# Optimization experiments

Hardware: AMD Instinct MI355X
Metric: run time of the kernel (lower is better)

## Reference

```python
import jax, jax.numpy as jnp
import numpy as np

B, S, H, NH = 8, 2048, 128, 4
HS = H // NH
EPS = 1e-8


def setup_inputs() -> dict:
    key = jax.random.key(0)
    ks = jax.random.split(key, 20)
    sc = 1.0 / np.sqrt(H)
    d = {
        'item_embeds': jax.random.normal(ks[0], (B, S, H), jnp.float32),
        'behavior_embeds': jax.random.normal(ks[1], (B, S, H), jnp.float32),
        'attn_mask': jnp.zeros((B, 1, S, S), jnp.float32),
    }
    names = ['Wq', 'Wk', 'Wv', 'Wqb', 'Wkb', 'Wvb', 'Wf']
    for i, n in enumerate(names):
        d[n] = jax.random.normal(ks[2 + i], (H, H), jnp.float32) * sc
        d['b' + n[1:]] = jnp.zeros((H,), jnp.float32)
    d['ln_w'] = jnp.ones((H,), jnp.float32)
    d['ln_b'] = jnp.zeros((H,), jnp.float32)
    return d


def _split_heads(x):
    # [B,S,H] -> [B,NH,S,HS]
    return x.reshape(B, S, NH, HS).transpose(0, 2, 1, 3)


def _layer_norm(x, w, b):
    u = jnp.mean(x, -1, keepdims=True)
    s = jnp.mean((x - u) ** 2, -1, keepdims=True)
    return w * ((x - u) / jnp.sqrt(s + EPS)) + b


def reference(item_embeds, behavior_embeds, attn_mask,
              Wq, bq, Wk, bk, Wv, bv,
              Wqb, bqb, Wkb, bkb, Wvb, bvb,
              Wf, bf, ln_w, ln_b):
    Q = _split_heads(item_embeds @ Wq + bq)
    K = _split_heads(item_embeds @ Wk + bk)
    V = _split_heads(item_embeds @ Wv + bv)
    Qb = _split_heads(behavior_embeds @ Wqb + bqb)
    Kb = _split_heads(behavior_embeds @ Wkb + bkb)
    # V_behavior computed in the original forward but unused downstream
    _Vb = _split_heads(behavior_embeds @ Wvb + bvb)
    scores = (jnp.einsum('bhqd,bhkd->bhqk', Q, K)
              + jnp.einsum('bhqd,bhkd->bhqk', Qb, Kb)) / np.sqrt(HS)
    scores = scores + attn_mask
    probs = jax.nn.softmax(scores, axis=-1)
    attn_out = jnp.einsum('bhqk,bhkd->bhqd', probs, V)
    attn_out = attn_out.transpose(0, 2, 1, 3).reshape(B, S, H)
    out = attn_out @ Wf + bf
    return _layer_norm(out + item_embeds, ln_w, ln_b)
```

## Files before the change

### kernel.cpp

```cpp
#include <hip/hip_runtime.h>
#include <math.h>

typedef unsigned short ushort_t;
typedef __attribute__((ext_vector_type(8))) short bf16x8;
typedef __attribute__((ext_vector_type(4))) float f32x4;

namespace {
constexpr int B = 8, S = 2048, H = 128, NH = 4, HS = 32;
constexpr float EPS = 1e-8f;
constexpr float SCALE = 0.17677669529663687f;
constexpr int QT = 16, KT = 64;
constexpr int NE = B * S * H;
}

__device__ __forceinline__ ushort_t f2bf(float f) {
  unsigned u = __float_as_uint(f);
  unsigned r = (u + 0x7FFFu + ((u >> 16) & 1u)) >> 16;
  return (ushort_t)r;
}

__device__ __forceinline__ f32x4 mfma16(bf16x8 a, bf16x8 b, f32x4 c) {
  return __builtin_amdgcn_mfma_f32_16x16x32_bf16(a, b, c, 0, 0, 0);
}

__global__ __launch_bounds__(256) void wcvt_kernel(
    const float* __restrict__ Wq, const float* __restrict__ Wk, const float* __restrict__ Wv,
    const float* __restrict__ Wqb, const float* __restrict__ Wkb, const float* __restrict__ Wf,
    ushort_t* __restrict__ Wt)
{
  const float* Ws[6] = {Wq, Wk, Wv, Wqb, Wkb, Wf};
  const float scl[6] = {SCALE, 1.f, 1.f, SCALE, 1.f, 1.f};
  const int m = blockIdx.y;
  const int kb = blockIdx.x;
  const float* W = Ws[m];
  const float sc = scl[m];
  __shared__ float T[32 * 132];
  const int t = threadIdx.x;
#pragma unroll
  for (int u = 0; u < 4; ++u) {
    const int idx = u * 256 + t;
    const int row = idx >> 5, c4 = idx & 31;
    const float4 v = *(const float4*)&W[(kb * 32 + row) * H + c4 * 4];
    *(float4*)&T[row * 132 + c4 * 4] = v;
  }
  __syncthreads();
#pragma unroll
  for (int u = 0; u < 16; ++u) {
    const int idx = u * 256 + t;
    const int n = idx >> 5, kk = idx & 31;
    Wt[m * (H * H) + n * H + kb * 32 + kk] = f2bf(T[kk * 132 + n] * sc);
  }
}

__global__ __launch_bounds__(256) void proj_kernel(
    const float* __restrict__ item, const float* __restrict__ beh,
    const ushort_t* __restrict__ Wt,
    const float* __restrict__ bq, const float* __restrict__ bk, const float* __restrict__ bv,
    const float* __restrict__ bqb, const float* __restrict__ bkb,
    ushort_t* __restrict__ Qo, ushort_t* __restrict__ Ko, ushort_t* __restrict__ Qbo,
    ushort_t* __restrict__ Kbo, ushort_t* __restrict__ Vto)
{
  __shared__ ushort_t Xi[16 * 136];
  __shared__ ushort_t Xb[16 * 136];
  __shared__ ushort_t Yb[5][16 * 136];
  const int t = threadIdx.x;
  const long r0 = (long)blockIdx.x * 16;
#pragma unroll
  for (int u = 0; u < 2; ++u) {
    const int idx = u * 256 + t;
    const int row = idx >> 5, c4 = idx & 31;
    const float4 vi = *(const float4*)&item[(r0 + row) * H + c4 * 4];
    const float4 vb = *(const float4*)&beh[(r0 + row) * H + c4 * 4];
    unsigned long long pi = (unsigned long long)f2bf(vi.x) | ((unsigned long long)f2bf(vi.y) << 16)
        | ((unsigned long long)f2bf(vi.z) << 32) | ((unsigned long long)f2bf(vi.w) << 48);
    unsigned long long pb = (unsigned long long)f2bf(vb.x) | ((unsigned long long)f2bf(vb.y) << 16)
        | ((unsigned long long)f2bf(vb.z) << 32) | ((unsigned long long)f2bf(vb.w) << 48);
    *(unsigned long long*)&Xi[row * 136 + c4 * 4] = pi;
    *(unsigned long long*)&Xb[row * 136 + c4 * 4] = pb;
  }
  __syncthreads();

  const int w = t >> 6, l = t & 63, l15 = l & 15, quad = l >> 4;
  const int bb = (int)(r0 >> 11);
  const int s0 = (int)(r0 & (S - 1));
  const float* bias[5] = {bq, bk, bv, bqb, bkb};
  const float bscale[5] = {SCALE, 1.f, 1.f, SCALE, 1.f};

  bf16x8 afi[4], afb[4];
#pragma unroll
  for (int ks = 0; ks < 4; ++ks) {
    afi[ks] = *(const bf16x8*)&Xi[l15 * 136 + ks * 32 + quad * 8];
    afb[ks] = *(const bf16x8*)&Xb[l15 * 136 + ks * 32 + quad * 8];
  }

#pragma unroll
  for (int p = 0; p < 5; ++p) {
    f32x4 acc[2];
#pragma unroll
    for (int nt = 0; nt < 2; ++nt) {
      const float bcol = bias[p][w * 32 + nt * 16 + l15] * bscale[p];
      acc[nt] = (f32x4){bcol, bcol, bcol, bcol};
    }
    const ushort_t* Wp = Wt + p * (H * H);
    const bf16x8* af = (p < 3) ? afi : afb;
#pragma unroll
    for (int ks = 0; ks < 4; ++ks) {
      bf16x8 bfr[2];
#pragma unroll
      for (int nt = 0; nt < 2; ++nt)
        bfr[nt] = *(const bf16x8*)&Wp[(w * 32 + nt * 16 + l15) * H + ks * 32 + quad * 8];
#pragma unroll
      for (int nt = 0; nt < 2; ++nt)
        acc[nt] = mfma16(af[ks], bfr[nt], acc[nt]);
    }
#pragma unroll
    for (int nt = 0; nt < 2; ++nt)
#pragma unroll
      for (int r = 0; r < 4; ++r)
        Yb[p][(quad * 4 + r) * 136 + w * 32 + nt * 16 + l15] = f2bf(acc[nt][r]);
  }
  __syncthreads();
  {
    const int row = t >> 4, cb = (t & 15) * 8;
    const int h = cb >> 5, dd = cb & 31;
    const long gidx = ((long)(bb * NH + h) * S + s0 + row) * HS + dd;
    ushort_t* dsts4[4] = {Qo, Ko, Qbo, Kbo};
    const int psrc[4] = {0, 1, 3, 4};
#pragma unroll
    for (int i = 0; i < 4; ++i)
      *(uint4*)&dsts4[i][gidx] = *(const uint4*)&Yb[psrc[i]][row * 136 + cb];
    const int d = t >> 1, sh = (t & 1) * 8;
    ushort_t tmp[8];
#pragma unroll
    for (int i = 0; i < 8; ++i) tmp[i] = Yb[2][(sh + i) * 136 + d];
    const long vidx = ((long)(bb * NH + (d >> 5)) * HS + (d & 31)) * S + s0 + sh;
    *(uint4*)&Vto[vidx] = *(const uint4*)&tmp[0];
  }
}

__global__ __launch_bounds__(256, 4) void attn_kernel(
    const ushort_t* __restrict__ Q, const ushort_t* __restrict__ K,
    const ushort_t* __restrict__ Qb, const ushort_t* __restrict__ Kb,
    const ushort_t* __restrict__ Vt, const float* __restrict__ mask,
    ushort_t* __restrict__ attn_out)
{
  __shared__ ushort_t Pb[NH][16 * 72];
  const int t = threadIdx.x;
  const int w = t >> 6;
  const int l = t & 63, l15 = l & 15, quad = l >> 4;
  const int q0 = blockIdx.x * QT;
  const int b = blockIdx.y;
  const long hQ = (long)(b * NH + w) * S * HS;
  const long hV = (long)(b * NH + w) * HS * S;

  const bf16x8 qf  = *(const bf16x8*)&Q[hQ + (long)(q0 + l15) * HS + quad * 8];
  const bf16x8 qbf = *(const bf16x8*)&Qb[hQ + (long)(q0 + l15) * HS + quad * 8];

  const float* mrow[4];
#pragma unroll
  for (int r = 0; r < 4; ++r)
    mrow[r] = mask + ((long)b * S + q0 + quad * 4 + r) * S + l15;

  float lsum[4] = {0.f, 0.f, 0.f, 0.f};
  f32x4 O[2];
#pragma unroll
  for (int dt = 0; dt < 2; ++dt) O[dt] = (f32x4){0.f, 0.f, 0.f, 0.f};
  ushort_t* Pw = Pb[w];

  float msk[4][4];
#pragma unroll
  for (int nt = 0; nt < 4; ++nt)
#pragma unroll
    for (int r = 0; r < 4; ++r)
      msk[nt][r] = mrow[r][nt * 16];

  for (int kt = 0; kt < S / KT; ++kt) {
    const int k0 = kt * KT;
    f32x4 sc[4];
#pragma unroll
    for (int nt = 0; nt < 4; ++nt)
#pragma unroll
      for (int r = 0; r < 4; ++r)
        sc[nt][r] = msk[nt][r];
    if (kt + 1 < S / KT) {
#pragma unroll
      for (int nt = 0; nt < 4; ++nt)
#pragma unroll
        for (int r = 0; r < 4; ++r)
          msk[nt][r] = mrow[r][k0 + KT + nt * 16];
    }
    bf16x8 kf[4], kbf[4], vf[2][2];
#pragma unroll
    for (int nt = 0; nt < 4; ++nt) {
      kf[nt]  = *(const bf16x8*)&K[hQ + (long)(k0 + nt * 16 + l15) * HS + quad * 8];
      kbf[nt] = *(const bf16x8*)&Kb[hQ + (long)(k0 + nt * 16 + l15) * HS + quad * 8];
    }
#pragma unroll
    for (int dt = 0; dt < 2; ++dt)
#pragma unroll
      for (int ks = 0; ks < 2; ++ks)
        vf[dt][ks] = *(const bf16x8*)&Vt[hV + (long)(dt * 16 + l15) * S + k0 + ks * 32 + quad * 8];
#pragma unroll
    for (int nt = 0; nt < 4; ++nt) {
      sc[nt] = mfma16(qbf, kbf[nt], sc[nt]);
      sc[nt] = mfma16(qf, kf[nt], sc[nt]);
    }
#pragma unroll
    for (int nt = 0; nt < 4; ++nt) {
      float ps = 0.f;
#pragma unroll
      for (int r = 0; r < 4; ++r) {
        const float p = __expf(sc[nt][r]);
        sc[nt][r] = p;
      }
      (void)ps;
    }
#pragma unroll
    for (int r = 0; r < 4; ++r)
      lsum[r] += sc[0][r] + sc[1][r] + sc[2][r] + sc[3][r];
#pragma unroll
    for (int nt = 0; nt < 4; ++nt)
#pragma unroll
      for (int r = 0; r < 4; ++r)
        Pw[(quad * 4 + r) * 72 + nt * 16 + l15] = f2bf(sc[nt][r]);
    bf16x8 pf[2];
#pragma unroll
    for (int ks = 0; ks < 2; ++ks)
      pf[ks] = *(const bf16x8*)&Pw[l15 * 72 + ks * 32 + quad * 8];
#pragma unroll
    for (int dt = 0; dt < 2; ++dt)
#pragma unroll
      for (int ks = 0; ks < 2; ++ks)
        O[dt] = mfma16(pf[ks], vf[dt][ks], O[dt]);
  }
#pragma unroll
  for (int r = 0; r < 4; ++r) {
    float s = lsum[r];
    s += __shfl_xor(s, 1);
    s += __shfl_xor(s, 2);
    s += __shfl_xor(s, 4);
    s += __shfl_xor(s, 8);
    lsum[r] = s;
  }
#pragma unroll
  for (int r = 0; r < 4; ++r) {
    const float inv = 1.f / lsum[r];
    const long row = (long)b * S + q0 + quad * 4 + r;
#pragma unroll
    for (int dt = 0; dt < 2; ++dt)
      attn_out[row * H + w * 32 + dt * 16 + l15] = f2bf(O[dt][r] * inv);
  }
}

__global__ __launch_bounds__(256) void out_kernel(
    const ushort_t* __restrict__ attn, const float* __restrict__ item,
    const ushort_t* __restrict__ Wft, const float* __restrict__ bf_,
    const float* __restrict__ lnw, const float* __restrict__ lnb,
    float* __restrict__ out)
{
  __shared__ ushort_t As[16 * 136];
  __shared__ float Ys[16 * 132];
  const int t = threadIdx.x;
  const long r0 = (long)blockIdx.x * 16;
  {
    const int row = t >> 4, c8 = t & 15;
    *(uint4*)&As[row * 136 + c8 * 8] = *(const uint4*)&attn[(r0 + row) * H + c8 * 8];
  }
  __syncthreads();
  const int w = t >> 6, l = t & 63, l15 = l & 15, quad = l >> 4;
  f32x4 acc[2];
#pragma unroll
  for (int nt = 0; nt < 2; ++nt) {
    const float bcol = bf_[w * 32 + nt * 16 + l15];
    acc[nt] = (f32x4){bcol, bcol, bcol, bcol};
  }
#pragma unroll
  for (int ks = 0; ks < 4; ++ks) {
    const bf16x8 a = *(const bf16x8*)&As[l15 * 136 + ks * 32 + quad * 8];
#pragma unroll
    for (int nt = 0; nt < 2; ++nt) {
      const bf16x8 bfr = *(const bf16x8*)&Wft[(w * 32 + nt * 16 + l15) * H + ks * 32 + quad * 8];
      acc[nt] = mfma16(a, bfr, acc[nt]);
    }
  }
#pragma unroll
  for (int nt = 0; nt < 2; ++nt)
#pragma unroll
    for (int r = 0; r < 4; ++r) {
      const int rl = quad * 4 + r;
      const int col = w * 32 + nt * 16 + l15;
      Ys[rl * 132 + col] = acc[nt][r] + item[(r0 + rl) * H + col];
    }
  __syncthreads();
  const int rl = t >> 4, ch = t & 15;
  float v[8];
#pragma unroll
  for (int g = 0; g < 2; ++g) {
    const float4 y = *(const float4*)&Ys[rl * 132 + ch * 8 + g * 4];
    v[g * 4 + 0] = y.x; v[g * 4 + 1] = y.y; v[g * 4 + 2] = y.z; v[g * 4 + 3] = y.w;
  }
  float s = 0.f;
#pragma unroll
  for (int i = 0; i < 8; ++i) s += v[i];
  s += __shfl_xor(s, 1);
  s += __shfl_xor(s, 2);
  s += __shfl_xor(s, 4);
  s += __shfl_xor(s, 8);
  const float u_ = s * (1.f / H);
  float s2 = 0.f;
#pragma unroll
  for (int i = 0; i < 8; ++i) { const float d = v[i] - u_; s2 += d * d; }
  s2 += __shfl_xor(s2, 1);
  s2 += __shfl_xor(s2, 2);
  s2 += __shfl_xor(s2, 4);
  s2 += __shfl_xor(s2, 8);
  const float rinv = rsqrtf(s2 * (1.f / H) + EPS);
#pragma unroll
  for (int g = 0; g < 2; ++g) {
    float4 o;
    const int col = ch * 8 + g * 4;
    o.x = lnw[col + 0] * ((v[g * 4 + 0] - u_) * rinv) + lnb[col + 0];
    o.y = lnw[col + 1] * ((v[g * 4 + 1] - u_) * rinv) + lnb[col + 1];
    o.z = lnw[col + 2] * ((v[g * 4 + 2] - u_) * rinv) + lnb[col + 2];
    o.w = lnw[col + 3] * ((v[g * 4 + 3] - u_) * rinv) + lnb[col + 3];
    *(float4*)&out[(r0 + rl) * H + col] = o;
  }
}

extern "C" void kernel_launch(void* const* d_in, const int* in_sizes, int n_in,
                              void* d_out, int out_size, void* d_ws, size_t ws_size,
                              hipStream_t stream) {
  const float* item = (const float*)d_in[0];
  const float* beh  = (const float*)d_in[1];
  const float* mask = (const float*)d_in[2];
  const float* Wq  = (const float*)d_in[3];  const float* bq  = (const float*)d_in[4];
  const float* Wk  = (const float*)d_in[5];  const float* bk  = (const float*)d_in[6];
  const float* Wv  = (const float*)d_in[7];  const float* bv  = (const float*)d_in[8];
  const float* Wqb = (const float*)d_in[9];  const float* bqb = (const float*)d_in[10];
  const float* Wkb = (const float*)d_in[11]; const float* bkb = (const float*)d_in[12];
  const float* Wf  = (const float*)d_in[15]; const float* bfv = (const float*)d_in[16];
  const float* lnw = (const float*)d_in[17]; const float* lnb = (const float*)d_in[18];
  float* out = (float*)d_out;

  ushort_t* ws = (ushort_t*)d_ws;
  ushort_t* Qw   = ws;
  ushort_t* Kw   = Qw + NE;
  ushort_t* Qbw  = Kw + NE;
  ushort_t* Kbw  = Qbw + NE;
  ushort_t* Vtw  = Kbw + NE;
  ushort_t* Attw = Vtw + NE;
  ushort_t* Wt   = Attw + NE;

  wcvt_kernel<<<dim3(4, 6), 256, 0, stream>>>(Wq, Wk, Wv, Wqb, Wkb, Wf, Wt);
  proj_kernel<<<dim3((B * S) / 16), 256, 0, stream>>>(
      item, beh, Wt, bq, bk, bv, bqb, bkb, Qw, Kw, Qbw, Kbw, Vtw);
  attn_kernel<<<dim3(S / QT, B), 256, 0, stream>>>(
      Qw, Kw, Qbw, Kbw, Vtw, mask, Attw);
  out_kernel<<<dim3((B * S) / 16), 256, 0, stream>>>(
      Attw, item, Wt + 5 * H * H, bfv, lnw, lnb, out);
}
```

Before: 394.0 us.

## Precompute per-tile mask nonzero flags and skip mask loads; double-buffer K fragments

```diff
diff --git a/kernel.cpp b/kernel.cpp
--- a/kernel.cpp
+++ b/kernel.cpp
@@ -21,6 +21,32 @@
 
 __device__ __forceinline__ f32x4 mfma16(bf16x8 a, bf16x8 b, f32x4 c) {
   return __builtin_amdgcn_mfma_f32_16x16x32_bf16(a, b, c, 0, 0, 0);
+}
+
+__global__ __launch_bounds__(256) void mflag_kernel(
+    const float* __restrict__ mask, unsigned* __restrict__ fm)
+{
+  const int qt = blockIdx.x;
+  const int b  = blockIdx.y;
+  const int t = threadIdx.x;
+  __shared__ unsigned fmask;
+  if (t == 0) fmask = 0u;
+  __syncthreads();
+  const float* mp = mask + ((long)b * S + (long)qt * QT) * S + t * 8;
+  float s = 0.f;
+#pragma unroll 4
+  for (int row = 0; row < QT; ++row) {
+    const float4 a = *(const float4*)&mp[(long)row * S];
+    const float4 c = *(const float4*)&mp[(long)row * S + 4];
+    s += fabsf(a.x) + fabsf(a.y) + fabsf(a.z) + fabsf(a.w)
+       + fabsf(c.x) + fabsf(c.y) + fabsf(c.z) + fabsf(c.w);
+  }
+  s += __shfl_xor(s, 1);
+  s += __shfl_xor(s, 2);
+  s += __shfl_xor(s, 4);
+  if ((t & 7) == 0 && !(s == 0.f)) atomicOr(&fmask, 1u << (t >> 3));
+  __syncthreads();
+  if (t == 0) fm[b * (S / QT) + qt] = fmask;
 }
 
 __global__ __launch_bounds__(256) void wcvt_kernel(
@@ -138,16 +164,79 @@
   }
 }
 
-__global__ __launch_bounds__(256, 4) void attn_kernel(
+__device__ __forceinline__ void attn_step(
+    int k0, int kn, bool msknz,
+    const bf16x8 (&kfc)[4], const bf16x8 (&kbfc)[4],
+    bf16x8 (&kfn)[4], bf16x8 (&kbfn)[4],
+    const bf16x8& qf, const bf16x8& qbf,
+    const ushort_t* __restrict__ K, const ushort_t* __restrict__ Kb,
+    const ushort_t* __restrict__ Vt,
+    long hQ, long hV, const float* const (&mrow)[4],
+    int l15, int quad, ushort_t* Pw,
+    float (&lsum)[4], f32x4 (&O)[2])
+{
+  bf16x8 vf[2][2];
+#pragma unroll
+  for (int dt = 0; dt < 2; ++dt)
+#pragma unroll
+    for (int ks = 0; ks < 2; ++ks)
+      vf[dt][ks] = *(const bf16x8*)&Vt[hV + (long)(dt * 16 + l15) * S + k0 + ks * 32 + quad * 8];
+#pragma unroll
+  for (int nt = 0; nt < 4; ++nt) {
+    kfn[nt]  = *(const bf16x8*)&K[hQ + (long)(kn + nt * 16 + l15) * HS + quad * 8];
+    kbfn[nt] = *(const bf16x8*)&Kb[hQ + (long)(kn + nt * 16 + l15) * HS + quad * 8];
+  }
+  f32x4 sc[4];
+  if (msknz) {
+#pragma unroll
+    for (int nt = 0; nt < 4; ++nt)
+#pragma unroll
+      for (int r = 0; r < 4; ++r)
+        sc[nt][r] = mrow[r][k0 + nt * 16];
+  } else {
+#pragma unroll
+    for (int nt = 0; nt < 4; ++nt)
+      sc[nt] = (f32x4){0.f, 0.f, 0.f, 0.f};
+  }
+#pragma unroll
+  for (int nt = 0; nt < 4; ++nt) {
+    sc[nt] = mfma16(qbf, kbfc[nt], sc[nt]);
+    sc[nt] = mfma16(qf, kfc[nt], sc[nt]);
+  }
+#pragma unroll
+  for (int nt = 0; nt < 4; ++nt)
+#pragma unroll
+    for (int r = 0; r < 4; ++r)
+      sc[nt][r] = __expf(sc[nt][r]);
+#pragma unroll
+  for (int r = 0; r < 4; ++r)
+    lsum[r] += sc[0][r] + sc[1][r] + sc[2][r] + sc[3][r];
+#pragma unroll
+  for (int nt = 0; nt < 4; ++nt)
+#pragma unroll
+    for (int r = 0; r < 4; ++r)
+      Pw[(quad * 4 + r) * 72 + nt * 16 + l15] = f2bf(sc[nt][r]);
+  bf16x8 pf[2];
+#pragma unroll
+  for (int ks = 0; ks < 2; ++ks)
+    pf[ks] = *(const bf16x8*)&Pw[l15 * 72 + ks * 32 + quad * 8];
+#pragma unroll
+  for (int dt = 0; dt < 2; ++dt)
+#pragma unroll
+    for (int ks = 0; ks < 2; ++ks)
+      O[dt] = mfma16(pf[ks], vf[dt][ks], O[dt]);
+}
+
+__global__ __launch_bounds__(256, 3) void attn_kernel(
     const ushort_t* __restrict__ Q, const ushort_t* __restrict__ K,
     const ushort_t* __restrict__ Qb, const ushort_t* __restrict__ Kb,
     const ushort_t* __restrict__ Vt, const float* __restrict__ mask,
-    ushort_t* __restrict__ attn_out)
+    const unsigned* __restrict__ fmg, ushort_t* __restrict__ attn_out)
 {
   __shared__ ushort_t Pb[NH][16 * 72];
   const int t = threadIdx.x;
   const int w = t >> 6;
-  const int l = t & 63, l15 = l & 15, quad = l >> 4;
+  const int l15 = t & 15, quad = (t & 63) >> 4;
   const int q0 = blockIdx.x * QT;
   const int b = blockIdx.y;
   const long hQ = (long)(b * NH + w) * S * HS;
@@ -156,6 +245,8 @@
   const bf16x8 qf  = *(const bf16x8*)&Q[hQ + (long)(q0 + l15) * HS + quad * 8];
   const bf16x8 qbf = *(const bf16x8*)&Qb[hQ + (long)(q0 + l15) * HS + quad * 8];
 
+  const unsigned fm = fmg[b * (S / QT) + blockIdx.x];
+
   const float* mrow[4];
 #pragma unroll
   for (int r = 0; r < 4; ++r)
@@ -167,71 +258,21 @@
   for (int dt = 0; dt < 2; ++dt) O[dt] = (f32x4){0.f, 0.f, 0.f, 0.f};
   ushort_t* Pw = Pb[w];
 
-  float msk[4][4];
-#pragma unroll
-  for (int nt = 0; nt < 4; ++nt)
-#pragma unroll
-    for (int r = 0; r < 4; ++r)
-      msk[nt][r] = mrow[r][nt * 16];
-
-  for (int kt = 0; kt < S / KT; ++kt) {
+  bf16x8 kfA[4], kbfA[4], kfB[4], kbfB[4];
+#pragma unroll
+  for (int nt = 0; nt < 4; ++nt) {
+    kfA[nt]  = *(const bf16x8*)&K[hQ + (long)(nt * 16 + l15) * HS + quad * 8];
+    kbfA[nt] = *(const bf16x8*)&Kb[hQ + (long)(nt * 16 + l15) * HS + quad * 8];
+  }
+
+  for (int kt = 0; kt < S / KT; kt += 2) {
     const int k0 = kt * KT;
-    f32x4 sc[4];
-#pragma unroll
-    for (int nt = 0; nt < 4; ++nt)
-#pragma unroll
-      for (int r = 0; r < 4; ++r)
-        sc[nt][r] = msk[nt][r];
-    if (kt + 1 < S / KT) {
-#pragma unroll
-      for (int nt = 0; nt < 4; ++nt)
-#pragma unroll
-        for (int r = 0; r < 4; ++r)
-          msk[nt][r] = mrow[r][k0 + KT + nt * 16];
-    }
-    bf16x8 kf[4], kbf[4], vf[2][2];
-#pragma unroll
-    for (int nt = 0; nt < 4; ++nt) {
-      kf[nt]  = *(const bf16x8*)&K[hQ + (long)(k0 + nt * 16 + l15) * HS + quad * 8];
-      kbf[nt] = *(const bf16x8*)&Kb[hQ + (long)(k0 + nt * 16 + l15) * HS + quad * 8];
-    }
-#pragma unroll
-    for (int dt = 0; dt < 2; ++dt)
-#pragma unroll
-      for (int ks = 0; ks < 2; ++ks)
-        vf[dt][ks] = *(const bf16x8*)&Vt[hV + (long)(dt * 16 + l15) * S + k0 + ks * 32 + quad * 8];
-#pragma unroll
-    for (int nt = 0; nt < 4; ++nt) {
-      sc[nt] = mfma16(qbf, kbf[nt], sc[nt]);
-      sc[nt] = mfma16(qf, kf[nt], sc[nt]);
-    }
-#pragma unroll
-    for (int nt = 0; nt < 4; ++nt) {
-      float ps = 0.f;
-#pragma unroll
-      for (int r = 0; r < 4; ++r) {
-        const float p = __expf(sc[nt][r]);
-        sc[nt][r] = p;
-      }
-      (void)ps;
-    }
-#pragma unroll
-    for (int r = 0; r < 4; ++r)
-      lsum[r] += sc[0][r] + sc[1][r] + sc[2][r] + sc[3][r];
-#pragma unroll
-    for (int nt = 0; nt < 4; ++nt)
-#pragma unroll
-      for (int r = 0; r < 4; ++r)
-        Pw[(quad * 4 + r) * 72 + nt * 16 + l15] = f2bf(sc[nt][r]);
-    bf16x8 pf[2];
-#pragma unroll
-    for (int ks = 0; ks < 2; ++ks)
-      pf[ks] = *(const bf16x8*)&Pw[l15 * 72 + ks * 32 + quad * 8];
-#pragma unroll
-    for (int dt = 0; dt < 2; ++dt)
-#pragma unroll
-      for (int ks = 0; ks < 2; ++ks)
-        O[dt] = mfma16(pf[ks], vf[dt][ks], O[dt]);
+    const int kn1 = k0 + KT;
+    const int kn2 = (kt + 2 < S / KT) ? k0 + 2 * KT : k0;
+    attn_step(k0, kn1, (fm >> kt) & 1u, kfA, kbfA, kfB, kbfB,
+              qf, qbf, K, Kb, Vt, hQ, hV, mrow, l15, quad, Pw, lsum, O);
+    attn_step(kn1, kn2, (fm >> (kt + 1)) & 1u, kfB, kbfB, kfA, kbfA,
+              qf, qbf, K, Kb, Vt, hQ, hV, mrow, l15, quad, Pw, lsum, O);
   }
 #pragma unroll
   for (int r = 0; r < 4; ++r) {
@@ -267,7 +308,7 @@
     *(uint4*)&As[row * 136 + c8 * 8] = *(const uint4*)&attn[(r0 + row) * H + c8 * 8];
   }
   __syncthreads();
-  const int w = t >> 6, l = t & 63, l15 = l & 15, quad = l >> 4;
+  const int w = t >> 6, l15 = t & 15, quad = (t & 63) >> 4;
   f32x4 acc[2];
 #pragma unroll
   for (int nt = 0; nt < 2; ++nt) {
@@ -350,12 +391,14 @@
   ushort_t* Vtw  = Kbw + NE;
   ushort_t* Attw = Vtw + NE;
   ushort_t* Wt   = Attw + NE;
-
+  unsigned* fm   = (unsigned*)(Wt + 6 * H * H);
+
+  mflag_kernel<<<dim3(S / QT, B), 256, 0, stream>>>(mask, fm);
   wcvt_kernel<<<dim3(4, 6), 256, 0, stream>>>(Wq, Wk, Wv, Wqb, Wkb, Wf, Wt);
   proj_kernel<<<dim3((B * S) / 16), 256, 0, stream>>>(
       item, beh, Wt, bq, bk, bv, bqb, bkb, Qw, Kw, Qbw, Kbw, Vtw);
   attn_kernel<<<dim3(S / QT, B), 256, 0, stream>>>(
-      Qw, Kw, Qbw, Kbw, Vtw, mask, Attw);
+      Qw, Kw, Qbw, Kbw, Vtw, mask, fm, Attw);
   out_kernel<<<dim3((B * S) / 16), 256, 0, stream>>>(
       Attw, item, Wt + 5 * H * H, bfv, lnw, lnb, out);
 }
```

After: 390.4 us. About the same (-0.9%).
